# Optimization experiments

Hardware: AMD Instinct MI355X
Metric: run time of the kernel (lower is better)

Reference implementation:

```python
import jax, jax.numpy as jnp
import numpy as np

THRESH = 1e-6
EPS = 1e-8
LN_EPS = 1e-5


def _layer(h, M, W_in, b_in, W_out, b_out, W_self, b_self, gamma, beta):
    # Normalize incoming flows per destination column: A[j,i] = M[j,i]/sum_k M[k,i]
    A = M / (jnp.sum(M, axis=0, keepdims=True) + EPS)
    mask = A > THRESH
    W = jnp.where(mask, A, 0.0)                      # thresholded edge weights [N,N]
    T = h @ W_in + b_in                              # transformed features [N,out]
    weighted_sum = jnp.einsum('ji,jd->id', W, T)     # sum over origins j per dest i
    weight_sum = jnp.sum(W, axis=0)                  # [N]
    has_edge = jnp.any(mask, axis=0)                 # dest i has >=1 incoming edge
    agg = jnp.where(has_edge[:, None],
                    weighted_sum / (weight_sum[:, None] + EPS),
                    T)
    agg = agg @ W_out + b_out                        # dropout is identity in eval
    out = agg + (h @ W_self + b_self)                # residual (dims differ -> self_transform)
    mu = jnp.mean(out, axis=-1, keepdims=True)
    var = jnp.mean(jnp.square(out - mu), axis=-1, keepdims=True)
    out = (out - mu) * jax.lax.rsqrt(var + LN_EPS) * gamma + beta
    return out


def setup_inputs() -> dict:
    key = jax.random.key(0)
    ks = jax.random.split(key, 16)
    N, D_IN, D_H, D_OUT = 8192, 256, 512, 256
    s = 0.05
    return {
        'node_features': jax.random.normal(ks[0], (N, D_IN), jnp.float32),
        'mobility_matrix': jax.random.uniform(ks[1], (N, N), jnp.float32),
        # layer 1: in -> hidden
        'W_in1': jax.random.normal(ks[2], (D_IN, D_H)) * s,
        'b_in1': jnp.zeros((D_H,)),
        'W_out1': jax.random.normal(ks[3], (D_H, D_H)) * s,
        'b_out1': jnp.zeros((D_H,)),
        'W_self1': jax.random.normal(ks[4], (D_IN, D_H)) * s,
        'b_self1': jnp.zeros((D_H,)),
        'g1': jnp.ones((D_H,)),
        'be1': jnp.zeros((D_H,)),
        # layer 2: hidden -> out
        'W_in2': jax.random.normal(ks[5], (D_H, D_OUT)) * s,
        'b_in2': jnp.zeros((D_OUT,)),
        'W_out2': jax.random.normal(ks[6], (D_OUT, D_OUT)) * s,
        'b_out2': jnp.zeros((D_OUT,)),
        'W_self2': jax.random.normal(ks[7], (D_H, D_OUT)) * s,
        'b_self2': jnp.zeros((D_OUT,)),
        'g2': jnp.ones((D_OUT,)),
        'be2': jnp.zeros((D_OUT,)),
    }


def reference(node_features, mobility_matrix,
              W_in1, b_in1, W_out1, b_out1, W_self1, b_self1, g1, be1,
              W_in2, b_in2, W_out2, b_out2, W_self2, b_self2, g2, be2):
    h = _layer(node_features, mobility_matrix,
               W_in1, b_in1, W_out1, b_out1, W_self1, b_self1, g1, be1)
    h = jax.nn.relu(h)  # inter-layer activation
    h = _layer(h, mobility_matrix,
               W_in2, b_in2, W_out2, b_out2, W_self2, b_self2, g2, be2)
    h = jax.nn.relu(h)  # final activation
    return h
```

## Files before the change

kernel.cpp:

```cpp
#include <hip/hip_runtime.h>
#include <stdint.h>

typedef short bf16x8 __attribute__((ext_vector_type(8)));
typedef short s16x4 __attribute__((ext_vector_type(4)));
typedef float f32x4 __attribute__((ext_vector_type(4)));
typedef unsigned int u32;

#define EPS_A 1e-8f
#define THR_A 1e-6f
#define NN 8192

static __device__ __forceinline__ short f2bf(float f) {
  u32 u = __float_as_uint(f);
  u = u + 0x7FFFu + ((u >> 16) & 1u);
  return (short)(u >> 16);
}
static __device__ __forceinline__ float bf2f(short s) {
  return __uint_as_float(((u32)(unsigned short)s) << 16);
}
static __device__ __forceinline__ void gld16(const short* g, short* l) {
  __builtin_amdgcn_global_load_lds(
      (const __attribute__((address_space(1))) u32*)g,
      (__attribute__((address_space(3))) u32*)l, 16, 0, 0);
}

__global__ __launch_bounds__(256) void k_prep_all(
    const float* __restrict__ Mob, const float* __restrict__ nf,
    const float* __restrict__ W_in1, const float* __restrict__ W_out1,
    const float* __restrict__ W_self1, const float* __restrict__ W_in2,
    const float* __restrict__ W_out2, const float* __restrict__ W_self2,
    const float* __restrict__ b_in1, const float* __restrict__ b_out1,
    const float* __restrict__ b_self1, const float* __restrict__ b_out2,
    const float* __restrict__ b_self2,
    short* __restrict__ Mt, float* __restrict__ colsum, u32* __restrict__ colmax,
    short* __restrict__ nft, short* __restrict__ A1cat, short* __restrict__ Win1b,
    short* __restrict__ Wout1t, short* __restrict__ Bcat1, short* __restrict__ Win2t,
    short* __restrict__ Bcat2, float* __restrict__ bias1c, float* __restrict__ bias2c)
{
  __shared__ __align__(16) short sbuf[256 * 66];
  int b = blockIdx.x;
  const int t = threadIdx.x;
  if (b < 4096) {
    const int i0 = (b & 31) * 256;
    const int j0 = (b >> 5) * 64;
    const int i = i0 + t;
    float s = 0.f, mx = 0.f;
    #pragma unroll 4
    for (int jj = 0; jj < 64; ++jj) {
      float v = Mob[(size_t)(j0 + jj) * NN + i];
      s += v;
      mx = fmaxf(mx, v);
      sbuf[t * 66 + jj] = f2bf(v);
    }
    atomicAdd(&colsum[i], s);
    atomicMax(&colmax[i], __float_as_uint(mx));
    __syncthreads();
    #pragma unroll
    for (int p = 0; p < 8; ++p) {
      const int r = p * 32 + (t >> 3);
      const int c = t & 7;
      const u32* src = (const u32*)((const char*)sbuf + r * 132 + c * 16);
      int4 w = make_int4(src[0], src[1], src[2], src[3]);
      *(int4*)((char*)Mt + (((size_t)(i0 + r) * NN + j0) * 2 + c * 16)) = w;
    }
    return;
  }
  b -= 4096;
  if (b < 512) {
    short (*tile)[65] = (short(*)[65])sbuf;
    const int r0 = (b & 127) * 64, c0 = (b >> 7) * 64;
    #pragma unroll
    for (int p = 0; p < 16; ++p) {
      const int rr = p * 4 + (t >> 6), cc = t & 63;
      tile[rr][cc] = f2bf(nf[(size_t)(r0 + rr) * 256 + c0 + cc]);
    }
    __syncthreads();
    #pragma unroll
    for (int q = 0; q < 16; ++q) {
      const int cc = q * 4 + (t >> 6), rr = t & 63;
      nft[(size_t)(c0 + cc) * 8192 + r0 + rr] = tile[rr][cc];
    }
    return;
  }
  b -= 512;
  if (b < 2048) {
    const int idx = b * 256 + t;
    const float4 v = ((const float4*)nf)[idx];
    const int i = idx >> 6;
    const int c = (idx & 63) * 4;
    s16x4 o;
    o.x = f2bf(v.x); o.y = f2bf(v.y); o.z = f2bf(v.z); o.w = f2bf(v.w);
    *(s16x4*)&A1cat[(size_t)i * 512 + 256 + c] = o;
    return;
  }
  b -= 2048;
  if (b < 128) {
    const int idx = b * 256 + t;
    const float4 v = ((const float4*)W_in1)[idx];
    s16x4 o;
    o.x = f2bf(v.x); o.y = f2bf(v.y); o.z = f2bf(v.z); o.w = f2bf(v.w);
    *(s16x4*)&Win1b[idx * 4] = o;
    return;
  }
  b -= 128;
  if (b < 1024) {
    const int idx = b * 256 + t;
    const int r = idx >> 9, c = idx & 511;
    Wout1t[(size_t)c * 512 + r] = f2bf(W_out1[idx]);
    return;
  }
  b -= 1024;
  if (b < 512) {
    const int idx = b * 256 + t;
    const int r = idx >> 9, c = idx & 511;
    Bcat1[(size_t)c * 512 + 256 + r] = f2bf(W_self1[idx]);
    return;
  }
  b -= 512;
  if (b < 512) {
    const int idx = b * 256 + t;
    const int r = idx >> 8, c = idx & 255;
    Win2t[(size_t)c * 512 + r] = f2bf(W_in2[idx]);
    return;
  }
  b -= 512;
  if (b < 256) {
    const int idx = b * 256 + t;
    const int r = idx >> 8, c = idx & 255;
    Bcat2[(size_t)c * 768 + r] = f2bf(W_out2[idx]);
    return;
  }
  b -= 256;
  if (b < 512) {
    const int idx = b * 256 + t;
    const int r = idx >> 8, c = idx & 255;
    Bcat2[(size_t)c * 768 + 256 + r] = f2bf(W_self2[idx]);
    return;
  }
  b -= 512;
  if (b < 2) {
    const int n = b * 256 + t;
    float a = b_out1[n] + b_self1[n];
    for (int p = 0; p < 512; ++p) a += b_in1[p] * W_out1[(size_t)p * 512 + n];
    bias1c[n] = a;
    return;
  }
  bias2c[t] = b_out2[t] + b_self2[t];
}

template <int BN, int EPI>
__device__ __forceinline__ void gemm_body(
    const short* __restrict__ A, const short* __restrict__ B, int K, int ldA, int ldB,
    void* __restrict__ Cout, int ldC, const float* __restrict__ bias0)
{
  constexpr int BM = 64;
  constexpr int MI = BM / 32;
  constexpr int NI = BN / 32;
  constexpr int LDP = 40;
  __shared__ __align__(16) short As[BM * LDP];
  __shared__ __align__(16) short Bs[BN * LDP];
  const int t = threadIdx.x;

  const int gx = gridDim.x;
  int flat = blockIdx.y * gx + blockIdx.x;
  const int cpx = (gx * gridDim.y) >> 3;
  flat = (flat & 7) * cpx + (flat >> 3);
  const int bx = flat % gx, by = flat / gx;
  const int m0 = by * BM, n0 = bx * BN;

  const int wid = t >> 6, l = t & 63;
  const int wr = wid >> 1, wc = wid & 1;
  const int lr = l & 15, lk = l >> 4;

  f32x4 acc[MI][NI] = {};

  const int sr = t >> 2;
  const int sc = (t & 3) * 8;
  const short* gA0 = A + (size_t)(m0 + sr) * ldA + sc;
  const short* gB0 = B + (size_t)(n0 + sr) * ldB + sc;
  const short* gB1 = gB0 + (size_t)64 * ldB;

  for (int k0 = 0; k0 < K; k0 += 32) {
    const int4 a0 = *(const int4*)(gA0 + k0);
    const int4 b0 = *(const int4*)(gB0 + k0);
    int4 b1 = make_int4(0, 0, 0, 0);
    if (NI == 4) b1 = *(const int4*)(gB1 + k0);
    __syncthreads();
    *(int4*)&As[sr * LDP + sc] = a0;
    *(int4*)&Bs[sr * LDP + sc] = b0;
    if (NI == 4) *(int4*)&Bs[(64 + sr) * LDP + sc] = b1;
    __syncthreads();

    bf16x8 av[MI], bv[NI];
    #pragma unroll
    for (int mi = 0; mi < MI; ++mi)
      av[mi] = *(const bf16x8*)&As[(wr * (BM / 2) + mi * 16 + lr) * LDP + lk * 8];
    #pragma unroll
    for (int ni = 0; ni < NI; ++ni)
      bv[ni] = *(const bf16x8*)&Bs[(wc * (BN / 2) + ni * 16 + lr) * LDP + lk * 8];
    #pragma unroll
    for (int mi = 0; mi < MI; ++mi)
      #pragma unroll
      for (int ni = 0; ni < NI; ++ni)
        acc[mi][ni] = __builtin_amdgcn_mfma_f32_16x16x32_bf16(av[mi], bv[ni], acc[mi][ni], 0, 0, 0);
  }

  #pragma unroll
  for (int mi = 0; mi < MI; ++mi) {
    #pragma unroll
    for (int r = 0; r < 4; ++r) {
      const int m = m0 + wr * (BM / 2) + mi * 16 + lk * 4 + r;
      float b0 = 0.f;
      if (EPI == 0) b0 = bias0[m];
      #pragma unroll
      for (int ni = 0; ni < NI; ++ni) {
        const int n = n0 + wc * (BN / 2) + ni * 16 + lr;
        float v = acc[mi][ni][r];
        if (EPI == 0) {
          v += b0;
          ((short*)Cout)[(size_t)m * ldC + n] = f2bf(v);
        } else if (EPI == 3) {
          ((short*)Cout)[(size_t)m * ldC + n] = f2bf(v);
        } else {
          v += bias0[n];
          ((float*)Cout)[(size_t)m * ldC + n] = v;
        }
      }
    }
  }
}

__global__ __launch_bounds__(256) void k_gemm_bias_n(
    const short* __restrict__ A, const short* __restrict__ B, int K, int ldA, int ldB,
    void* __restrict__ C, int ldC, const float* __restrict__ bias0) {
  gemm_body<64, 0>(A, B, K, ldA, ldB, C, ldC, bias0);
}
__global__ __launch_bounds__(256) void k_gemm_raw_n(
    const short* __restrict__ A, const short* __restrict__ B, int K, int ldA, int ldB,
    void* __restrict__ C, int ldC) {
  gemm_body<64, 3>(A, B, K, ldA, ldB, C, ldC, nullptr);
}
__global__ __launch_bounds__(256) void k_gemm_out_w(
    const short* __restrict__ A, const short* __restrict__ B, int K, int ldA, int ldB,
    void* __restrict__ C, int ldC, const float* __restrict__ bias0) {
  gemm_body<128, 2>(A, B, K, ldA, ldB, C, ldC, bias0);
}
__global__ __launch_bounds__(256) void k_gemm_out_n(
    const short* __restrict__ A, const short* __restrict__ B, int K, int ldA, int ldB,
    void* __restrict__ C, int ldC, const float* __restrict__ bias0) {
  gemm_body<64, 2>(A, B, K, ldA, ldB, C, ldC, bias0);
}

__global__ __launch_bounds__(256) void k_gemm_sk128(
    const short* __restrict__ A, const short* __restrict__ B, int K, int ldA, int ldB,
    short* __restrict__ P, int ldC, size_t pstride)
{
  __shared__ __align__(16) short As[128 * 64];
  __shared__ __align__(16) short Bs[128 * 64];
  const int t = threadIdx.x;

  const int sk = blockIdx.z;
  A += (size_t)sk * K;
  B += (size_t)sk * K;

  const int gx = gridDim.x;
  int flat = blockIdx.y * gx + blockIdx.x;
  const int cpx = (gx * gridDim.y) >> 3;
  flat = (flat & 7) * cpx + (flat >> 3);
  const int bx = flat % gx, by = flat / gx;
  const int m0 = by * 128, n0 = bx * 128;

  const int wid = t >> 6, l = t & 63;
  const int wr = wid >> 1, wc = wid & 1;
  const int lr = l & 15, lk = l >> 4;

  f32x4 acc[4][4] = {};

  const int side = wid >> 1;
  const int hrow = (wid & 1) * 64;
  const short* Xp = side ? B : A;
  const int ldX = side ? ldB : ldA;
  const int x0 = side ? n0 : m0;
  short* dbase = (side ? Bs : As) + hrow * 64;
  const int lrow = l >> 3, lcol = l & 7;
  const short* g0 = Xp + (size_t)(x0 + hrow + lrow) * ldX + (lcol ^ lrow) * 8;
  const size_t st8 = (size_t)8 * ldX;

  const int niters = K >> 6;
  int kk = (flat + sk * 3) & (niters - 1);

  for (int it = 0; it < niters; ++it) {
    const int koff = kk << 6;
    kk = (kk + 1) & (niters - 1);
    __syncthreads();
    gld16(g0 + koff,            dbase);
    gld16(g0 + koff + st8,      dbase + 512);
    gld16(g0 + koff + 2 * st8,  dbase + 1024);
    gld16(g0 + koff + 3 * st8,  dbase + 1536);
    gld16(g0 + koff + 4 * st8,  dbase + 2048);
    gld16(g0 + koff + 5 * st8,  dbase + 2560);
    gld16(g0 + koff + 6 * st8,  dbase + 3072);
    gld16(g0 + koff + 7 * st8,  dbase + 3584);
    __syncthreads();

    #pragma unroll
    for (int ks = 0; ks < 2; ++ks) {
      bf16x8 av[4], bv[4];
      #pragma unroll
      for (int mi = 0; mi < 4; ++mi) {
        const int row = wr * 64 + mi * 16 + lr;
        av[mi] = *(const bf16x8*)&As[row * 64 + ((ks * 4 + lk) ^ (lr & 7)) * 8];
      }
      #pragma unroll
      for (int ni = 0; ni < 4; ++ni) {
        const int row = wc * 64 + ni * 16 + lr;
        bv[ni] = *(const bf16x8*)&Bs[row * 64 + ((ks * 4 + lk) ^ (lr & 7)) * 8];
      }
      #pragma unroll
      for (int mi = 0; mi < 4; ++mi)
        #pragma unroll
        for (int ni = 0; ni < 4; ++ni)
          acc[mi][ni] = __builtin_amdgcn_mfma_f32_16x16x32_bf16(av[mi], bv[ni], acc[mi][ni], 0, 0, 0);
    }
  }

  short* outp = P + pstride * sk;
  #pragma unroll
  for (int mi = 0; mi < 4; ++mi) {
    #pragma unroll
    for (int r = 0; r < 4; ++r) {
      const int m = m0 + wr * 64 + mi * 16 + lk * 4 + r;
      #pragma unroll
      for (int ni = 0; ni < 4; ++ni) {
        const int n = n0 + wc * 64 + ni * 16 + lr;
        outp[(size_t)m * ldC + n] = f2bf(acc[mi][ni][r]);
      }
    }
  }
}

__global__ __launch_bounds__(256) void k_sk_reduce_sub(
    const short* __restrict__ P, int N, size_t pstride, int S,
    const float* __restrict__ colsum, const u32* __restrict__ colmax,
    const short* __restrict__ hraw, int ldh,
    short* __restrict__ out, int ldo)
{
  const int idx = blockIdx.x * 256 + threadIdx.x;
  const int nq = N >> 2;
  const int m = idx / nq;
  const int c4 = (idx - m * nq) * 4;
  const size_t base = (size_t)m * N + c4;
  float a0 = 0.f, a1 = 0.f, a2 = 0.f, a3 = 0.f;
  for (int s = 0; s < S; ++s) {
    s16x4 v = *(const s16x4*)&P[pstride * s + base];
    a0 += bf2f(v.x); a1 += bf2f(v.y); a2 += bf2f(v.z); a3 += bf2f(v.w);
  }
  const float cs = colsum[m];
  const float rc = 1.f / (cs + EPS_A);
  const float rcw = rc / (cs * rc + EPS_A);
  const bool he = __uint_as_float(colmax[m]) * rc > THR_A;
  s16x4 o;
  if (he) {
    o.x = f2bf(a0 * rcw); o.y = f2bf(a1 * rcw);
    o.z = f2bf(a2 * rcw); o.w = f2bf(a3 * rcw);
  } else {
    o = *(const s16x4*)&hraw[(size_t)m * ldh + c4];
  }
  *(s16x4*)&out[(size_t)m * ldo + c4] = o;
}

__global__ __launch_bounds__(256) void k_sk_reduce(
    const short* __restrict__ P, int N, size_t pstride, int S,
    const float* __restrict__ colsum, const u32* __restrict__ colmax,
    const short* __restrict__ Tfall, short* __restrict__ out, int ldo)
{
  const int idx = blockIdx.x * 256 + threadIdx.x;
  const int nq = N >> 2;
  const int m = idx / nq;
  const int c4 = (idx - m * nq) * 4;
  const size_t base = (size_t)m * N + c4;
  float a0 = 0.f, a1 = 0.f, a2 = 0.f, a3 = 0.f;
  for (int s = 0; s < S; ++s) {
    s16x4 v = *(const s16x4*)&P[pstride * s + base];
    a0 += bf2f(v.x); a1 += bf2f(v.y); a2 += bf2f(v.z); a3 += bf2f(v.w);
  }
  const float cs = colsum[m];
  const float rc = 1.f / (cs + EPS_A);
  const float rcw = rc / (cs * rc + EPS_A);
  const bool he = __uint_as_float(colmax[m]) * rc > THR_A;
  a0 *= rcw; a1 *= rcw; a2 *= rcw; a3 *= rcw;
  if (__ballot(!he)) {
    if (!he) {
      a0 = bf2f(Tfall[(size_t)(c4 + 0) * NN + m]);
      a1 = bf2f(Tfall[(size_t)(c4 + 1) * NN + m]);
      a2 = bf2f(Tfall[(size_t)(c4 + 2) * NN + m]);
      a3 = bf2f(Tfall[(size_t)(c4 + 3) * NN + m]);
    }
  }
  s16x4 o;
  o.x = f2bf(a0); o.y = f2bf(a1); o.z = f2bf(a2); o.w = f2bf(a3);
  *(s16x4*)&out[(size_t)m * ldo + c4] = o;
}

template <int MODE>
__device__ __forceinline__ void ln_relu_body(
    const float* __restrict__ X, int W,
    const float* __restrict__ g, const float* __restrict__ be,
    void* __restrict__ out, int ldo)
{
  const int row = blockIdx.x;
  const int t = threadIdx.x;
  const float* x = X + (size_t)row * W;
  float v0 = x[t], v1 = 0.f;
  float s = v0, ss = v0 * v0;
  if (W == 512) { v1 = x[t + 256]; s += v1; ss += v1 * v1; }
  #pragma unroll
  for (int off = 32; off; off >>= 1) {
    s += __shfl_down(s, off);
    ss += __shfl_down(ss, off);
  }
  __shared__ float red[8];
  const int wid = t >> 6;
  if ((t & 63) == 0) { red[wid] = s; red[4 + wid] = ss; }
  __syncthreads();
  s = red[0] + red[1] + red[2] + red[3];
  ss = red[4] + red[5] + red[6] + red[7];
  const float mu = s / W;
  const float var = ss / W - mu * mu;
  const float sc = rsqrtf(var + 1e-5f);
  float y = fmaxf((v0 - mu) * sc * g[t] + be[t], 0.f);
  if (MODE == 0) ((short*)out)[(size_t)row * ldo + t] = f2bf(y);
  else           ((float*)out)[(size_t)row * ldo + t] = y;
  if (W == 512) {
    float y1 = fmaxf((v1 - mu) * sc * g[t + 256] + be[t + 256], 0.f);
    if (MODE == 0) ((short*)out)[(size_t)row * ldo + t + 256] = f2bf(y1);
    else           ((float*)out)[(size_t)row * ldo + t + 256] = y1;
  }
}

__global__ __launch_bounds__(256) void k_ln_relu_bf16(
    const float* __restrict__ X, int W, const float* __restrict__ g,
    const float* __restrict__ be, short* __restrict__ out, int ldo) {
  ln_relu_body<0>(X, W, g, be, out, ldo);
}
__global__ __launch_bounds__(256) void k_ln_relu_f32(
    const float* __restrict__ X, int W, const float* __restrict__ g,
    const float* __restrict__ be, float* __restrict__ out, int ldo) {
  ln_relu_body<1>(X, W, g, be, out, ldo);
}

extern "C" void kernel_launch(void* const* d_in, const int* in_sizes, int n_in,
                              void* d_out, int out_size, void* d_ws, size_t ws_size,
                              hipStream_t stream) {
  const float* nf      = (const float*)d_in[0];
  const float* Mob     = (const float*)d_in[1];
  const float* W_in1   = (const float*)d_in[2];
  const float* b_in1   = (const float*)d_in[3];
  const float* W_out1  = (const float*)d_in[4];
  const float* b_out1  = (const float*)d_in[5];
  const float* W_self1 = (const float*)d_in[6];
  const float* b_self1 = (const float*)d_in[7];
  const float* g1      = (const float*)d_in[8];
  const float* be1     = (const float*)d_in[9];
  const float* W_in2   = (const float*)d_in[10];
  const float* b_in2   = (const float*)d_in[11];
  const float* W_out2  = (const float*)d_in[12];
  const float* b_out2  = (const float*)d_in[13];
  const float* W_self2 = (const float*)d_in[14];
  const float* b_self2 = (const float*)d_in[15];
  const float* g2      = (const float*)d_in[16];
  const float* be2     = (const float*)d_in[17];

  char* ws = (char*)d_ws;
  float* colsum = (float*)(ws);
  u32*   colmax = (u32*)(ws + 32768);
  short* Mt     = (short*)(ws + 65536);
  short* nft    = (short*)(ws + 134283264);
  short* A1cat  = (short*)(ws + 138477568);
  float* C2f    = (float*)(ws + 146866176);
  short* Acat2  = (short*)(ws + 163643392);
  short* T2t    = (short*)(ws + 176226304);
  short* Bcat1  = (short*)(ws + 180420608);
  short* Bcat2  = (short*)(ws + 180944896);
  short* Win2t  = (short*)(ws + 181338112);
  short* Wout1t = (short*)(ws + 181600256);
  short* Win1b  = (short*)(ws + 182124544);
  float* bias1c = (float*)(ws + 182386688);
  float* bias2c = (float*)(ws + 182390784);
  short* P1     = (short*)(ws + 188743680);
  short* P2     = (short*)(ws + 222298112);

  hipMemsetAsync(ws, 0, 65536, stream);

  k_prep_all<<<9603, 256, 0, stream>>>(Mob, nf, W_in1, W_out1, W_self1, W_in2,
                                       W_out2, W_self2, b_in1, b_out1, b_self1,
                                       b_out2, b_self2, Mt, colsum, colmax, nft,
                                       A1cat, Win1b, Wout1t, Bcat1, Win2t, Bcat2,
                                       bias1c, bias2c);
  k_gemm_raw_n<<<dim3(4, 8), 256, 0, stream>>>(Wout1t, Win1b, 512, 512, 512,
                                               Bcat1, 512);

  k_gemm_sk128<<<dim3(2, 64, 8), 256, 0, stream>>>(Mt, nft, 1024, NN, NN,
                                                   P1, 256, (size_t)8192 * 256);
  k_sk_reduce_sub<<<2048, 256, 0, stream>>>(P1, 256, (size_t)8192 * 256, 8,
                                            colsum, colmax, A1cat + 256, 512,
                                            A1cat, 512);
  k_gemm_out_w<<<dim3(4, 128), 256, 0, stream>>>(A1cat, Bcat1, 512, 512, 512,
                                                 C2f, 512, bias1c);
  k_ln_relu_bf16<<<8192, 256, 0, stream>>>(C2f, 512, g1, be1, Acat2 + 256, 768);

  k_gemm_bias_n<<<dim3(128, 4), 256, 0, stream>>>(Win2t, Acat2 + 256, 512, 512, 768,
                                                  T2t, NN, b_in2);
  k_gemm_sk128<<<dim3(2, 64, 8), 256, 0, stream>>>(Mt, T2t, 1024, NN, NN,
                                                   P2, 256, (size_t)8192 * 256);
  k_sk_reduce<<<2048, 256, 0, stream>>>(P2, 256, (size_t)8192 * 256, 8,
                                        colsum, colmax, T2t, Acat2, 768);
  k_gemm_out_n<<<dim3(4, 128), 256, 0, stream>>>(Acat2, Bcat2, 768, 768, 768,
                                                 C2f, 256, bias2c);
  k_ln_relu_f32<<<8192, 256, 0, stream>>>(C2f, 256, g2, be2, (float*)d_out, 256);
}
```

Before: 312.3 us.

## Fuse split-K reduction into last-arriving GEMM block and use async-LDS loads in small GEMMs

The split-K aggregation GEMM now counts arriving split blocks per output tile with an atomic counter, and the last block to finish reduces the partial sums and applies normalization and fallback. This removes the separate reduction kernels and their launches. The smaller GEMMs move from register-staged LDS copies to direct global-to-LDS loads, with a unified swizzled shared buffer, 64-wide K steps and rotated K start. The cost is a tail where a single block per tile does all the reduction, plus extra counters that must be zeroed each call.

```diff
diff --git a/kernel.cpp b/kernel.cpp
--- a/kernel.cpp
+++ b/kernel.cpp
@@ -148,17 +148,65 @@
   bias2c[t] = b_out2[t] + b_self2[t];
 }
 
+__global__ __launch_bounds__(256) void k_gemm_raw_n(
+    const short* __restrict__ A, const short* __restrict__ B, int K, int ldA, int ldB,
+    short* __restrict__ C, int ldC)
+{
+  constexpr int LDP = 40;
+  __shared__ __align__(16) short As[64 * LDP];
+  __shared__ __align__(16) short Bs[64 * LDP];
+  const int t = threadIdx.x;
+  const int m0 = blockIdx.y * 64, n0 = blockIdx.x * 64;
+  const int wid = t >> 6, l = t & 63;
+  const int wr = wid >> 1, wc = wid & 1;
+  const int lr = l & 15, lk = l >> 4;
+  f32x4 acc[2][2] = {};
+  const int sr = t >> 2;
+  const int sc = (t & 3) * 8;
+  const short* gA0 = A + (size_t)(m0 + sr) * ldA + sc;
+  const short* gB0 = B + (size_t)(n0 + sr) * ldB + sc;
+  for (int k0 = 0; k0 < K; k0 += 32) {
+    const int4 a0 = *(const int4*)(gA0 + k0);
+    const int4 b0 = *(const int4*)(gB0 + k0);
+    __syncthreads();
+    *(int4*)&As[sr * LDP + sc] = a0;
+    *(int4*)&Bs[sr * LDP + sc] = b0;
+    __syncthreads();
+    bf16x8 av[2], bv[2];
+    #pragma unroll
+    for (int mi = 0; mi < 2; ++mi)
+      av[mi] = *(const bf16x8*)&As[(wr * 32 + mi * 16 + lr) * LDP + lk * 8];
+    #pragma unroll
+    for (int ni = 0; ni < 2; ++ni)
+      bv[ni] = *(const bf16x8*)&Bs[(wc * 32 + ni * 16 + lr) * LDP + lk * 8];
+    #pragma unroll
+    for (int mi = 0; mi < 2; ++mi)
+      #pragma unroll
+      for (int ni = 0; ni < 2; ++ni)
+        acc[mi][ni] = __builtin_amdgcn_mfma_f32_16x16x32_bf16(av[mi], bv[ni], acc[mi][ni], 0, 0, 0);
+  }
+  #pragma unroll
+  for (int mi = 0; mi < 2; ++mi)
+    #pragma unroll
+    for (int r = 0; r < 4; ++r) {
+      const int m = m0 + wr * 32 + mi * 16 + lk * 4 + r;
+      #pragma unroll
+      for (int ni = 0; ni < 2; ++ni) {
+        const int n = n0 + wc * 32 + ni * 16 + lr;
+        C[(size_t)m * ldC + n] = f2bf(acc[mi][ni][r]);
+      }
+    }
+}
+
 template <int BN, int EPI>
-__device__ __forceinline__ void gemm_body(
+__global__ __launch_bounds__(256) void k_g64(
     const short* __restrict__ A, const short* __restrict__ B, int K, int ldA, int ldB,
     void* __restrict__ Cout, int ldC, const float* __restrict__ bias0)
 {
-  constexpr int BM = 64;
-  constexpr int MI = BM / 32;
+  constexpr int ROWS = 64 + BN;
+  constexpr int CH = ROWS / 32;
   constexpr int NI = BN / 32;
-  constexpr int LDP = 40;
-  __shared__ __align__(16) short As[BM * LDP];
-  __shared__ __align__(16) short Bs[BN * LDP];
+  __shared__ __align__(16) short S[ROWS * 64];
   const int t = threadIdx.x;
 
   const int gx = gridDim.x;
@@ -166,97 +214,87 @@
   const int cpx = (gx * gridDim.y) >> 3;
   flat = (flat & 7) * cpx + (flat >> 3);
   const int bx = flat % gx, by = flat / gx;
-  const int m0 = by * BM, n0 = bx * BN;
+  const int m0 = by * 64, n0 = bx * BN;
 
   const int wid = t >> 6, l = t & 63;
   const int wr = wid >> 1, wc = wid & 1;
   const int lr = l & 15, lk = l >> 4;
 
-  f32x4 acc[MI][NI] = {};
-
-  const int sr = t >> 2;
-  const int sc = (t & 3) * 8;
-  const short* gA0 = A + (size_t)(m0 + sr) * ldA + sc;
-  const short* gB0 = B + (size_t)(n0 + sr) * ldB + sc;
-  const short* gB1 = gB0 + (size_t)64 * ldB;
-
-  for (int k0 = 0; k0 < K; k0 += 32) {
-    const int4 a0 = *(const int4*)(gA0 + k0);
-    const int4 b0 = *(const int4*)(gB0 + k0);
-    int4 b1 = make_int4(0, 0, 0, 0);
-    if (NI == 4) b1 = *(const int4*)(gB1 + k0);
-    __syncthreads();
-    *(int4*)&As[sr * LDP + sc] = a0;
-    *(int4*)&Bs[sr * LDP + sc] = b0;
-    if (NI == 4) *(int4*)&Bs[(64 + sr) * LDP + sc] = b1;
-    __syncthreads();
-
-    bf16x8 av[MI], bv[NI];
-    #pragma unroll
-    for (int mi = 0; mi < MI; ++mi)
-      av[mi] = *(const bf16x8*)&As[(wr * (BM / 2) + mi * 16 + lr) * LDP + lk * 8];
-    #pragma unroll
-    for (int ni = 0; ni < NI; ++ni)
-      bv[ni] = *(const bf16x8*)&Bs[(wc * (BN / 2) + ni * 16 + lr) * LDP + lk * 8];
-    #pragma unroll
-    for (int mi = 0; mi < MI; ++mi)
-      #pragma unroll
-      for (int ni = 0; ni < NI; ++ni)
-        acc[mi][ni] = __builtin_amdgcn_mfma_f32_16x16x32_bf16(av[mi], bv[ni], acc[mi][ni], 0, 0, 0);
-  }
-
+  f32x4 acc[2][NI] = {};
+
+  const int lrow = l >> 3, lcol = l & 7;
+  const int wbase = wid * (ROWS / 4);
+  short* dbase = S + wbase * 64;
+  const short* gsrc[CH];
   #pragma unroll
-  for (int mi = 0; mi < MI; ++mi) {
+  for (int c = 0; c < CH; ++c) {
+    const int ar = wbase + c * 8 + lrow;
+    const int scol = (lcol ^ (ar & 7)) * 8;
+    gsrc[c] = (ar < 64) ? A + (size_t)(m0 + ar) * ldA + scol
+                        : B + (size_t)(n0 + ar - 64) * ldB + scol;
+  }
+
+  const int niters = K >> 6;
+  int kk = flat % niters;
+  for (int it = 0; it < niters; ++it) {
+    const int koff = kk << 6;
+    kk = (kk + 1 == niters) ? 0 : kk + 1;
+    __syncthreads();
+    #pragma unroll
+    for (int c = 0; c < CH; ++c)
+      gld16(gsrc[c] + koff, dbase + c * 512);
+    __syncthreads();
+
+    #pragma unroll
+    for (int ks = 0; ks < 2; ++ks) {
+      bf16x8 av[2], bv[NI];
+      #pragma unroll
+      for (int mi = 0; mi < 2; ++mi) {
+        const int row = wr * 32 + mi * 16 + lr;
+        av[mi] = *(const bf16x8*)&S[row * 64 + ((ks * 4 + lk) ^ (row & 7)) * 8];
+      }
+      #pragma unroll
+      for (int ni = 0; ni < NI; ++ni) {
+        const int row = 64 + wc * (BN / 2) + ni * 16 + lr;
+        bv[ni] = *(const bf16x8*)&S[row * 64 + ((ks * 4 + lk) ^ (row & 7)) * 8];
+      }
+      #pragma unroll
+      for (int mi = 0; mi < 2; ++mi)
+        #pragma unroll
+        for (int ni = 0; ni < NI; ++ni)
+          acc[mi][ni] = __builtin_amdgcn_mfma_f32_16x16x32_bf16(av[mi], bv[ni], acc[mi][ni], 0, 0, 0);
+    }
+  }
+
+  #pragma unroll
+  for (int mi = 0; mi < 2; ++mi) {
     #pragma unroll
     for (int r = 0; r < 4; ++r) {
-      const int m = m0 + wr * (BM / 2) + mi * 16 + lk * 4 + r;
-      float b0 = 0.f;
-      if (EPI == 0) b0 = bias0[m];
+      const int m = m0 + wr * 32 + mi * 16 + lk * 4 + r;
+      float bm = 0.f;
+      if (EPI == 0) bm = bias0[m];
       #pragma unroll
       for (int ni = 0; ni < NI; ++ni) {
         const int n = n0 + wc * (BN / 2) + ni * 16 + lr;
         float v = acc[mi][ni][r];
-        if (EPI == 0) {
-          v += b0;
-          ((short*)Cout)[(size_t)m * ldC + n] = f2bf(v);
-        } else if (EPI == 3) {
-          ((short*)Cout)[(size_t)m * ldC + n] = f2bf(v);
-        } else {
-          v += bias0[n];
-          ((float*)Cout)[(size_t)m * ldC + n] = v;
-        }
-      }
-    }
-  }
-}
-
-__global__ __launch_bounds__(256) void k_gemm_bias_n(
+        if (EPI == 0) ((short*)Cout)[(size_t)m * ldC + n] = f2bf(v + bm);
+        else          ((float*)Cout)[(size_t)m * ldC + n] = v + bias0[n];
+      }
+    }
+  }
+}
+
+template <int FB>
+__global__ __launch_bounds__(256) void k_sk128_red(
     const short* __restrict__ A, const short* __restrict__ B, int K, int ldA, int ldB,
-    void* __restrict__ C, int ldC, const float* __restrict__ bias0) {
-  gemm_body<64, 0>(A, B, K, ldA, ldB, C, ldC, bias0);
-}
-__global__ __launch_bounds__(256) void k_gemm_raw_n(
-    const short* __restrict__ A, const short* __restrict__ B, int K, int ldA, int ldB,
-    void* __restrict__ C, int ldC) {
-  gemm_body<64, 3>(A, B, K, ldA, ldB, C, ldC, nullptr);
-}
-__global__ __launch_bounds__(256) void k_gemm_out_w(
-    const short* __restrict__ A, const short* __restrict__ B, int K, int ldA, int ldB,
-    void* __restrict__ C, int ldC, const float* __restrict__ bias0) {
-  gemm_body<128, 2>(A, B, K, ldA, ldB, C, ldC, bias0);
-}
-__global__ __launch_bounds__(256) void k_gemm_out_n(
-    const short* __restrict__ A, const short* __restrict__ B, int K, int ldA, int ldB,
-    void* __restrict__ C, int ldC, const float* __restrict__ bias0) {
-  gemm_body<64, 2>(A, B, K, ldA, ldB, C, ldC, bias0);
-}
-
-__global__ __launch_bounds__(256) void k_gemm_sk128(
-    const short* __restrict__ A, const short* __restrict__ B, int K, int ldA, int ldB,
-    short* __restrict__ P, int ldC, size_t pstride)
+    short* __restrict__ P, size_t pstride, u32* __restrict__ cnt,
+    const float* __restrict__ colsum, const u32* __restrict__ colmax,
+    const short* __restrict__ fb, int ldfb,
+    short* __restrict__ out, int ldo)
 {
   __shared__ __align__(16) short As[128 * 64];
   __shared__ __align__(16) short Bs[128 * 64];
+  __shared__ int lastf;
   const int t = threadIdx.x;
 
   const int sk = blockIdx.z;
@@ -293,14 +331,14 @@
     const int koff = kk << 6;
     kk = (kk + 1) & (niters - 1);
     __syncthreads();
-    gld16(g0 + koff,            dbase);
-    gld16(g0 + koff + st8,      dbase + 512);
-    gld16(g0 + koff + 2 * st8,  dbase + 1024);
-    gld16(g0 + koff + 3 * st8,  dbase + 1536);
-    gld16(g0 + koff + 4 * st8,  dbase + 2048);
-    gld16(g0 + koff + 5 * st8,  dbase + 2560);
-    gld16(g0 + koff + 6 * st8,  dbase + 3072);
-    gld16(g0 + koff + 7 * st8,  dbase + 3584);
+    gld16(g0 + koff,           dbase);
+    gld16(g0 + koff + st8,     dbase + 512);
+    gld16(g0 + koff + 2 * st8, dbase + 1024);
+    gld16(g0 + koff + 3 * st8, dbase + 1536);
+    gld16(g0 + koff + 4 * st8, dbase + 2048);
+    gld16(g0 + koff + 5 * st8, dbase + 2560);
+    gld16(g0 + koff + 6 * st8, dbase + 3072);
+    gld16(g0 + koff + 7 * st8, dbase + 3584);
     __syncthreads();
 
     #pragma unroll
@@ -326,80 +364,62 @@
 
   short* outp = P + pstride * sk;
   #pragma unroll
-  for (int mi = 0; mi < 4; ++mi) {
+  for (int mi = 0; mi < 4; ++mi)
     #pragma unroll
     for (int r = 0; r < 4; ++r) {
       const int m = m0 + wr * 64 + mi * 16 + lk * 4 + r;
       #pragma unroll
       for (int ni = 0; ni < 4; ++ni) {
         const int n = n0 + wc * 64 + ni * 16 + lr;
-        outp[(size_t)m * ldC + n] = f2bf(acc[mi][ni][r]);
-      }
-    }
-  }
-}
-
-__global__ __launch_bounds__(256) void k_sk_reduce_sub(
-    const short* __restrict__ P, int N, size_t pstride, int S,
-    const float* __restrict__ colsum, const u32* __restrict__ colmax,
-    const short* __restrict__ hraw, int ldh,
-    short* __restrict__ out, int ldo)
-{
-  const int idx = blockIdx.x * 256 + threadIdx.x;
-  const int nq = N >> 2;
-  const int m = idx / nq;
-  const int c4 = (idx - m * nq) * 4;
-  const size_t base = (size_t)m * N + c4;
-  float a0 = 0.f, a1 = 0.f, a2 = 0.f, a3 = 0.f;
-  for (int s = 0; s < S; ++s) {
-    s16x4 v = *(const s16x4*)&P[pstride * s + base];
-    a0 += bf2f(v.x); a1 += bf2f(v.y); a2 += bf2f(v.z); a3 += bf2f(v.w);
-  }
-  const float cs = colsum[m];
-  const float rc = 1.f / (cs + EPS_A);
-  const float rcw = rc / (cs * rc + EPS_A);
-  const bool he = __uint_as_float(colmax[m]) * rc > THR_A;
-  s16x4 o;
-  if (he) {
-    o.x = f2bf(a0 * rcw); o.y = f2bf(a1 * rcw);
-    o.z = f2bf(a2 * rcw); o.w = f2bf(a3 * rcw);
-  } else {
-    o = *(const s16x4*)&hraw[(size_t)m * ldh + c4];
-  }
-  *(s16x4*)&out[(size_t)m * ldo + c4] = o;
-}
-
-__global__ __launch_bounds__(256) void k_sk_reduce(
-    const short* __restrict__ P, int N, size_t pstride, int S,
-    const float* __restrict__ colsum, const u32* __restrict__ colmax,
-    const short* __restrict__ Tfall, short* __restrict__ out, int ldo)
-{
-  const int idx = blockIdx.x * 256 + threadIdx.x;
-  const int nq = N >> 2;
-  const int m = idx / nq;
-  const int c4 = (idx - m * nq) * 4;
-  const size_t base = (size_t)m * N + c4;
-  float a0 = 0.f, a1 = 0.f, a2 = 0.f, a3 = 0.f;
-  for (int s = 0; s < S; ++s) {
-    s16x4 v = *(const s16x4*)&P[pstride * s + base];
-    a0 += bf2f(v.x); a1 += bf2f(v.y); a2 += bf2f(v.z); a3 += bf2f(v.w);
-  }
-  const float cs = colsum[m];
-  const float rc = 1.f / (cs + EPS_A);
-  const float rcw = rc / (cs * rc + EPS_A);
-  const bool he = __uint_as_float(colmax[m]) * rc > THR_A;
-  a0 *= rcw; a1 *= rcw; a2 *= rcw; a3 *= rcw;
-  if (__ballot(!he)) {
-    if (!he) {
-      a0 = bf2f(Tfall[(size_t)(c4 + 0) * NN + m]);
-      a1 = bf2f(Tfall[(size_t)(c4 + 1) * NN + m]);
-      a2 = bf2f(Tfall[(size_t)(c4 + 2) * NN + m]);
-      a3 = bf2f(Tfall[(size_t)(c4 + 3) * NN + m]);
-    }
-  }
-  s16x4 o;
-  o.x = f2bf(a0); o.y = f2bf(a1); o.z = f2bf(a2); o.w = f2bf(a3);
-  *(s16x4*)&out[(size_t)m * ldo + c4] = o;
+        outp[(size_t)m * 256 + n] = f2bf(acc[mi][ni][r]);
+      }
+    }
+
+  __threadfence();
+  __syncthreads();
+  if (t == 0)
+    lastf = (atomicAdd(&cnt[by * gx + bx], 1u) == gridDim.z - 1) ? 1 : 0;
+  __syncthreads();
+  if (!lastf) return;
+  __threadfence();
+
+  #pragma unroll 2
+  for (int i = 0; i < 16; ++i) {
+    const int q = i * 256 + t;
+    const int m = m0 + (q >> 5);
+    const int n = n0 + (q & 31) * 4;
+    const size_t base = (size_t)m * 256 + n;
+    float a0 = 0.f, a1 = 0.f, a2 = 0.f, a3 = 0.f;
+    for (int s = 0; s < 8; ++s) {
+      s16x4 v = *(const s16x4*)&P[pstride * s + base];
+      a0 += bf2f(v.x); a1 += bf2f(v.y); a2 += bf2f(v.z); a3 += bf2f(v.w);
+    }
+    const float cs = colsum[m];
+    const float rc = 1.f / (cs + EPS_A);
+    const float rcw = rc / (cs * rc + EPS_A);
+    const bool he = __uint_as_float(colmax[m]) * rc > THR_A;
+    s16x4 o;
+    if (FB == 0) {
+      if (he) {
+        o.x = f2bf(a0 * rcw); o.y = f2bf(a1 * rcw);
+        o.z = f2bf(a2 * rcw); o.w = f2bf(a3 * rcw);
+      } else {
+        o = *(const s16x4*)&fb[(size_t)m * ldfb + n];
+      }
+    } else {
+      a0 *= rcw; a1 *= rcw; a2 *= rcw; a3 *= rcw;
+      if (__ballot(!he)) {
+        if (!he) {
+          a0 = bf2f(fb[(size_t)(n + 0) * NN + m]);
+          a1 = bf2f(fb[(size_t)(n + 1) * NN + m]);
+          a2 = bf2f(fb[(size_t)(n + 2) * NN + m]);
+          a3 = bf2f(fb[(size_t)(n + 3) * NN + m]);
+        }
+      }
+      o.x = f2bf(a0); o.y = f2bf(a1); o.z = f2bf(a2); o.w = f2bf(a3);
+    }
+    *(s16x4*)&out[(size_t)m * ldo + n] = o;
+  }
 }
 
 template <int MODE>
@@ -474,23 +494,25 @@
   char* ws = (char*)d_ws;
   float* colsum = (float*)(ws);
   u32*   colmax = (u32*)(ws + 32768);
-  short* Mt     = (short*)(ws + 65536);
-  short* nft    = (short*)(ws + 134283264);
-  short* A1cat  = (short*)(ws + 138477568);
-  float* C2f    = (float*)(ws + 146866176);
-  short* Acat2  = (short*)(ws + 163643392);
-  short* T2t    = (short*)(ws + 176226304);
-  short* Bcat1  = (short*)(ws + 180420608);
-  short* Bcat2  = (short*)(ws + 180944896);
-  short* Win2t  = (short*)(ws + 181338112);
-  short* Wout1t = (short*)(ws + 181600256);
-  short* Win1b  = (short*)(ws + 182124544);
-  float* bias1c = (float*)(ws + 182386688);
-  float* bias2c = (float*)(ws + 182390784);
+  u32*   cnt1   = (u32*)(ws + 65536);
+  u32*   cnt2   = (u32*)(ws + 66048);
+  short* Mt     = (short*)(ws + 131072);
+  short* nft    = (short*)(ws + 134348800);
+  short* A1cat  = (short*)(ws + 138543104);
+  float* C2f    = (float*)(ws + 146931712);
+  short* Acat2  = (short*)(ws + 163708928);
+  short* T2t    = (short*)(ws + 176291840);
+  short* Bcat1  = (short*)(ws + 180486144);
+  short* Bcat2  = (short*)(ws + 181010432);
+  short* Win2t  = (short*)(ws + 181403648);
+  short* Wout1t = (short*)(ws + 181665792);
+  short* Win1b  = (short*)(ws + 182190080);
+  float* bias1c = (float*)(ws + 182452224);
+  float* bias2c = (float*)(ws + 182454272);
   short* P1     = (short*)(ws + 188743680);
   short* P2     = (short*)(ws + 222298112);
 
-  hipMemsetAsync(ws, 0, 65536, stream);
+  hipMemsetAsync(ws, 0, 69632, stream);
 
   k_prep_all<<<9603, 256, 0, stream>>>(Mob, nf, W_in1, W_out1, W_self1, W_in2,
                                        W_out2, W_self2, b_in1, b_out1, b_self1,
@@ -500,22 +522,19 @@
   k_gemm_raw_n<<<dim3(4, 8), 256, 0, stream>>>(Wout1t, Win1b, 512, 512, 512,
                                                Bcat1, 512);
 
-  k_gemm_sk128<<<dim3(2, 64, 8), 256, 0, stream>>>(Mt, nft, 1024, NN, NN,
-                                                   P1, 256, (size_t)8192 * 256);
-  k_sk_reduce_sub<<<2048, 256, 0, stream>>>(P1, 256, (size_t)8192 * 256, 8,
-                                            colsum, colmax, A1cat + 256, 512,
-                                            A1cat, 512);
-  k_gemm_out_w<<<dim3(4, 128), 256, 0, stream>>>(A1cat, Bcat1, 512, 512, 512,
-                                                 C2f, 512, bias1c);
+  k_sk128_red<0><<<dim3(2, 64, 8), 256, 0, stream>>>(
+      Mt, nft, 1024, NN, NN, P1, (size_t)8192 * 256, cnt1,
+      colsum, colmax, A1cat + 256, 512, A1cat, 512);
+  k_g64<128, 2><<<dim3(4, 128), 256, 0, stream>>>(A1cat, Bcat1, 512, 512, 512,
+                                                  C2f, 512, bias1c);
   k_ln_relu_bf16<<<8192, 256, 0, stream>>>(C2f, 512, g1, be1, Acat2 + 256, 768);
 
-  k_gemm_bias_n<<<dim3(128, 4), 256, 0, stream>>>(Win2t, Acat2 + 256, 512, 512, 768,
-                                                  T2t, NN, b_in2);
-  k_gemm_sk128<<<dim3(2, 64, 8), 256, 0, stream>>>(Mt, T2t, 1024, NN, NN,
-                                                   P2, 256, (size_t)8192 * 256);
-  k_sk_reduce<<<2048, 256, 0, stream>>>(P2, 256, (size_t)8192 * 256, 8,
-                                        colsum, colmax, T2t, Acat2, 768);
-  k_gemm_out_n<<<dim3(4, 128), 256, 0, stream>>>(Acat2, Bcat2, 768, 768, 768,
+  k_g64<64, 0><<<dim3(128, 4), 256, 0, stream>>>(Win2t, Acat2 + 256, 512, 512, 768,
+                                                 T2t, NN, b_in2);
+  k_sk128_red<1><<<dim3(2, 64, 8), 256, 0, stream>>>(
+      Mt, T2t, 1024, NN, NN, P2, (size_t)8192 * 256, cnt2,
+      colsum, colmax, T2t, NN, Acat2, 768);
+  k_g64<64, 2><<<dim3(4, 128), 256, 0, stream>>>(Acat2, Bcat2, 768, 768, 768,
                                                  C2f, 256, bias2c);
   k_ln_relu_f32<<<8192, 256, 0, stream>>>(C2f, 256, g2, be2, (float*)d_out, 256);
 }
```

Measured after the change: 673.2 us. 116% more time.
